# Optimization experiments

Measured on AMD Instinct MI355X. Metric: run time of the kernel, lower is better.

## Reference

```python
import jax, jax.numpy as jnp
import numpy as np

NUM_USERS = 120000
NUM_ITEMS = 30000
NUM_NODES = NUM_USERS + NUM_ITEMS
EMBED_DIM = 64
N_LAYERS = 3
N_EDGES = 4000000


def setup_inputs() -> dict:
    key = jax.random.key(0)
    k_emb, k_row, k_col = jax.random.split(key, 3)
    row = jax.random.randint(k_row, (N_EDGES,), 0, NUM_NODES, dtype=jnp.int32)
    col = jax.random.randint(k_col, (N_EDGES,), 0, NUM_NODES, dtype=jnp.int32)
    # symmetric normalization weights: D^{-1/2}[row] * D^{-1/2}[col]
    deg = jnp.bincount(row, length=NUM_NODES).astype(jnp.float32)
    deg_inv_sqrt = jnp.where(deg > 0, deg ** -0.5, 0.0)
    edge_weight = deg_inv_sqrt[row] * deg_inv_sqrt[col]
    emb = 0.1 * jax.random.normal(k_emb, (NUM_NODES, EMBED_DIM), dtype=jnp.float32)
    return {"emb": emb, "edge_weight": edge_weight, "row": row, "col": col}


def reference(emb, edge_weight, row, col):
    # one LightGCN propagation: out[row] += edge_weight * x[col]  (SpMM)
    def propagate(x):
        msg = x[col] * edge_weight[:, None]            # [E, D] gather + scale
        return jax.ops.segment_sum(msg, row, num_segments=NUM_NODES)  # scatter-add

    out = emb
    xk = emb
    for _ in range(N_LAYERS):
        xk = propagate(xk)
        out = out + xk
    out = out / (N_LAYERS + 1)
    user_emb = out[:NUM_USERS]
    item_emb = out[NUM_USERS:]
    return (user_emb, item_emb)
```

## Files before the change

### kernel.cpp

```cpp
#include <hip/hip_runtime.h>

#define NUM_USERS 120000
#define NUM_ITEMS 30000
#define NUM_NODES 150000
#define EMBED_DIM 64
#define N_LAYERS 3
#define N_EDGES 4000000

#define BW_SHIFT 9
#define BW_ROWS (1 << BW_SHIFT)
#define BW_MASK (BW_ROWS - 1)
#define NBUCK ((NUM_NODES + BW_MASK) >> BW_SHIFT)
#define BUCK_CAP 16000


__device__ __forceinline__ float bf2f(unsigned short u) {
    union { unsigned int i; float f; } v;
    v.i = ((unsigned int)u) << 16;
    return v.f;
}
__device__ __forceinline__ unsigned short f2bf(float f) {
    union { float f; unsigned int i; } v;
    v.f = f;
    unsigned int u = v.i;
    u += 0x7FFFu + ((u >> 16) & 1u);
    return (unsigned short)(u >> 16);
}


__global__ void zero_ints(int* __restrict__ p, int n) {
    int i = blockIdx.x * blockDim.x + threadIdx.x;
    int stride = gridDim.x * blockDim.x;
    for (; i < n; i += stride) p[i] = 0;
}

__global__ void conv_bf(const float4* __restrict__ src, ushort4* __restrict__ dst,
                        int n4) {
    int i = blockIdx.x * blockDim.x + threadIdx.x;
    int stride = gridDim.x * blockDim.x;
    for (; i < n4; i += stride) {
        float4 v = src[i];
        ushort4 q;
        q.x = f2bf(v.x); q.y = f2bf(v.y); q.z = f2bf(v.z); q.w = f2bf(v.w);
        dst[i] = q;
    }
}


__global__ void bucket_bin(const int* __restrict__ row, const int* __restrict__ col,
                           const float* __restrict__ w,
                           int* __restrict__ gcnt, int2* __restrict__ stage,
                           int nEdges) {
    __shared__ int cnt[NBUCK];
    __shared__ int bbase[NBUCK];
    int tile = (nEdges + gridDim.x - 1) / gridDim.x;
    int t0 = blockIdx.x * tile;
    int t1 = t0 + tile;
    if (t1 > nEdges) t1 = nEdges;
    for (int j = threadIdx.x; j < NBUCK; j += blockDim.x) cnt[j] = 0;
    __syncthreads();
    for (int i = t0 + threadIdx.x; i < t1; i += blockDim.x)
        atomicAdd(&cnt[row[i] >> BW_SHIFT], 1);
    __syncthreads();
    for (int j = threadIdx.x; j < NBUCK; j += blockDim.x) {
        int c = cnt[j];
        bbase[j] = c ? atomicAdd(&gcnt[j], c) : 0;
        cnt[j] = 0;
    }
    __syncthreads();
    for (int i = t0 + threadIdx.x; i < t1; i += blockDim.x) {
        int r = row[i];
        int b = r >> BW_SHIFT;
        int rank = bbase[b] + atomicAdd(&cnt[b], 1);
        if (rank < BUCK_CAP)
            stage[(size_t)b * BUCK_CAP + rank] =
                make_int2(((r & BW_MASK) << 18) | col[i], __float_as_int(w[i]));
    }
}

__global__ void bucket_scan(const int* __restrict__ gcnt, int* __restrict__ bstart,
                            int* __restrict__ rs) {
    __shared__ int s0[512], s1[512];
    int tid = threadIdx.x;
    int v = 0;
    if (tid < NBUCK) { v = gcnt[tid]; if (v > BUCK_CAP) v = BUCK_CAP; }
    s0[tid] = v;
    __syncthreads();
    int* a = s0; int* bb = s1;
    for (int off = 1; off < 512; off <<= 1) {
        int x = a[tid];
        if (tid >= off) x += a[tid - off];
        bb[tid] = x;
        __syncthreads();
        int* t = a; a = bb; bb = t;
    }
    if (tid == 0) bstart[0] = 0;
    if (tid < NBUCK) bstart[tid + 1] = a[tid];
    if (tid == 0) rs[NUM_NODES] = a[NBUCK - 1];
}

__global__ void __launch_bounds__(256)
bucket_scatter(const int2* __restrict__ stage, const int* __restrict__ gcnt,
               const int* __restrict__ bstart, int* __restrict__ rs,
               int2* __restrict__ csr) {
    __shared__ int s0[BW_ROWS], s1[BW_ROWS];
    int b = blockIdx.x;
    int tid = threadIdx.x;
    int nrec = gcnt[b]; if (nrec > BUCK_CAP) nrec = BUCK_CAP;
    int base = bstart[b];
    const int2* st = stage + (size_t)b * BUCK_CAP;
    int baseRow = b << BW_SHIFT;
    int rows = NUM_NODES - baseRow; if (rows > BW_ROWS) rows = BW_ROWS;

    for (int j = tid; j < BW_ROWS; j += 256) s0[j] = 0;
    __syncthreads();
    for (int i = tid; i < nrec; i += 256) atomicAdd(&s0[st[i].x >> 18], 1);
    __syncthreads();

    int* a = s0; int* bb = s1;
    for (int off = 1; off < BW_ROWS; off <<= 1) {
        for (int j = tid; j < BW_ROWS; j += 256) {
            int x = a[j];
            if (j >= off) x += a[j - off];
            bb[j] = x;
        }
        __syncthreads();
        int* t = a; a = bb; bb = t;
    }

    for (int r = tid; r < rows; r += 256)
        rs[baseRow + r] = base + (r ? a[r - 1] : 0);

    for (int j = tid; j < BW_ROWS; j += 256) bb[j] = 0;
    __syncthreads();
    for (int i = tid; i < nrec; i += 256) {
        int2 rec = st[i];
        int r = rec.x >> 18;
        int rank = atomicAdd(&bb[r], 1);
        csr[base + (r ? a[r - 1] : 0) + rank] = make_int2(rec.x & 0x3FFFF, rec.y);
    }
}

__global__ void lgcn_prop_bf(const ushort4* __restrict__ xb,
                             const int* __restrict__ rs,
                             const int2* __restrict__ csr,
                             ushort4* __restrict__ yb,
                             const float4* __restrict__ addIn,
                             float4* __restrict__ out,
                             float scale, int nNodes, int writeY) {
    int gtid = blockIdx.x * blockDim.x + threadIdx.x;
    int node = gtid >> 4;
    int sub  = threadIdx.x & 15;
    if (node >= nNodes) return;
    int s = rs[node], e = rs[node + 1];
    float4 acc = make_float4(0.f, 0.f, 0.f, 0.f);

    int base = s;
    for (; base + 16 <= e; base += 16) {
        int2 cw = csr[base + sub];
#pragma unroll
        for (int j = 0; j < 16; ++j) {
            int bc   = __shfl(cw.x, j, 16);
            float bw = __int_as_float(__shfl(cw.y, j, 16));
            ushort4 v = xb[(size_t)bc * 16 + sub];
            acc.x = fmaf(bf2f(v.x), bw, acc.x);
            acc.y = fmaf(bf2f(v.y), bw, acc.y);
            acc.z = fmaf(bf2f(v.z), bw, acc.z);
            acc.w = fmaf(bf2f(v.w), bw, acc.w);
        }
    }
    if (base < e) {
        int idx = base + sub;
        int2 cw = (idx < e) ? csr[idx] : make_int2(0, 0);
        int nn = e - base;
        for (int j = 0; j < nn; ++j) {
            int bc   = __shfl(cw.x, j, 16);
            float bw = __int_as_float(__shfl(cw.y, j, 16));
            ushort4 v = xb[(size_t)bc * 16 + sub];
            acc.x = fmaf(bf2f(v.x), bw, acc.x);
            acc.y = fmaf(bf2f(v.y), bw, acc.y);
            acc.z = fmaf(bf2f(v.z), bw, acc.z);
            acc.w = fmaf(bf2f(v.w), bw, acc.w);
        }
    }

    size_t o = (size_t)node * 16 + sub;
    if (writeY) {
        ushort4 q;
        q.x = f2bf(acc.x); q.y = f2bf(acc.y); q.z = f2bf(acc.z); q.w = f2bf(acc.w);
        yb[o] = q;
    }
    float4 a = addIn[o];
    a.x = (a.x + acc.x) * scale;
    a.y = (a.y + acc.y) * scale;
    a.z = (a.z + acc.z) * scale;
    a.w = (a.w + acc.w) * scale;
    out[o] = a;
}


__global__ void lgcn_init(const float4* __restrict__ emb,
                          float4* __restrict__ x,
                          float4* __restrict__ out, int n4) {
    int i = blockIdx.x * blockDim.x + threadIdx.x;
    int stride = gridDim.x * blockDim.x;
    for (; i < n4; i += stride) {
        float4 v = emb[i];
        x[i] = v;
        out[i] = v;
    }
}

__global__ void lgcn_zero(float4* __restrict__ y, int n4) {
    int i = blockIdx.x * blockDim.x + threadIdx.x;
    int stride = gridDim.x * blockDim.x;
    float4 z = make_float4(0.f, 0.f, 0.f, 0.f);
    for (; i < n4; i += stride) y[i] = z;
}

__global__ void lgcn_edge(const float* __restrict__ x,
                          const float* __restrict__ w,
                          const int* __restrict__ row,
                          const int* __restrict__ col,
                          float* __restrict__ y, int nEdges) {
    int tid = blockIdx.x * blockDim.x + threadIdx.x;
    int wave = tid >> 6;
    int lane = threadIdx.x & 63;
    int nWaves = (gridDim.x * blockDim.x) >> 6;
    for (int e = wave; e < nEdges; e += nWaves) {
        int r = row[e];
        int c = col[e];
        float wt = w[e];
        float v = x[(size_t)c * EMBED_DIM + lane] * wt;
        atomicAdd(&y[(size_t)r * EMBED_DIM + lane], v);
    }
}

__global__ void lgcn_accum(const float4* __restrict__ y,
                           float4* __restrict__ out, float scale, int n4) {
    int i = blockIdx.x * blockDim.x + threadIdx.x;
    int stride = gridDim.x * blockDim.x;
    for (; i < n4; i += stride) {
        float4 o = out[i];
        float4 v = y[i];
        o.x = (o.x + v.x) * scale;
        o.y = (o.y + v.y) * scale;
        o.z = (o.z + v.z) * scale;
        o.w = (o.w + v.w) * scale;
        out[i] = o;
    }
}


extern "C" void kernel_launch(void* const* d_in, const int* in_sizes, int n_in,
                              void* d_out, int out_size, void* d_ws, size_t ws_size,
                              hipStream_t stream) {
    const float* emb = (const float*)d_in[0];
    const float* ew  = (const float*)d_in[1];
    const int*   row = (const int*)d_in[2];
    const int*   col = (const int*)d_in[3];
    float* out = (float*)d_out;

    const size_t tableElems = (size_t)NUM_NODES * EMBED_DIM;
    const int n4 = (int)(tableElems / 4);

    char* ws = (char*)d_ws;
    size_t off = 0;
    auto alloc = [&](size_t bytes) {
        char* p = ws + off;
        off += (bytes + 255) & ~(size_t)255;
        return p;
    };
    ushort4* yAb   = (ushort4*)alloc(tableElems * 2);
    ushort4* yBb   = (ushort4*)alloc(tableElems * 2);
    int2*    csr   = (int2*)   alloc((size_t)N_EDGES * 8);
    int2*    stage = (int2*)   alloc((size_t)NBUCK * BUCK_CAP * 8);
    int*     rs    = (int*)    alloc((size_t)(NUM_NODES + 32) * 4);
    int*     bstart= (int*)    alloc((size_t)(NBUCK + 8) * 4);
    int*     gcnt  = (int*)    alloc((size_t)(NBUCK + 8) * 4);
    size_t need = off;
    ushort4* embb = (ushort4*)stage;

    if (ws_size >= need) {
        zero_ints<<<2, 256, 0, stream>>>(gcnt, NBUCK);
        bucket_bin<<<512, 256, 0, stream>>>(row, col, ew, gcnt, stage, N_EDGES);
        bucket_scan<<<1, 512, 0, stream>>>(gcnt, bstart, rs);
        bucket_scatter<<<NBUCK, 256, 0, stream>>>(stage, gcnt, bstart, rs, csr);

        conv_bf<<<2048, 256, 0, stream>>>((const float4*)emb, (ushort4*)embb, n4);

        const int propBlocks = (NUM_NODES * 16 + 255) / 256;
        lgcn_prop_bf<<<propBlocks, 256, 0, stream>>>(embb, rs, csr, yAb,
                                                     (const float4*)emb,
                                                     (float4*)out,
                                                     1.0f, NUM_NODES, 1);
        lgcn_prop_bf<<<propBlocks, 256, 0, stream>>>(yAb, rs, csr, yBb,
                                                     (const float4*)out,
                                                     (float4*)out,
                                                     1.0f, NUM_NODES, 1);
        lgcn_prop_bf<<<propBlocks, 256, 0, stream>>>(yBb, rs, csr, yAb,
                                                     (const float4*)out,
                                                     (float4*)out,
                                                     1.0f / (N_LAYERS + 1),
                                                     NUM_NODES, 0);
    } else {
        float* x = (float*)d_ws;
        float* y = x + tableElems;
        lgcn_init<<<2048, 256, 0, stream>>>((const float4*)emb, (float4*)x,
                                            (float4*)out, n4);
        for (int l = 0; l < N_LAYERS; ++l) {
            lgcn_zero<<<2048, 256, 0, stream>>>((float4*)y, n4);
            lgcn_edge<<<4096, 256, 0, stream>>>(x, ew, row, col, y, N_EDGES);
            float scale = (l == N_LAYERS - 1) ? 1.0f / (N_LAYERS + 1) : 1.0f;
            lgcn_accum<<<2048, 256, 0, stream>>>((const float4*)y, (float4*)out,
                                                 scale, n4);
            float* t = x; x = y; y = t;
        }
    }
}
```

Baseline: 377.6 us.

## Locally sort edges in shared memory, widen SpMM gathers, use nontemporal accesses

The binning kernel now processes 4096-edge sub-tiles, sorting them by bucket in shared memory via a local prefix scan, so writes to the staging buffer land in contiguous runs instead of being scattered. The propagation kernel uses 8 lanes per node with 16-byte bf16 gathers instead of 16 lanes with 8-byte gathers, which halves the shuffles and doubles the bytes per load. Streaming CSR, output and staging traffic switches to nontemporal loads and stores so the gathered embedding table stays in cache. In exchange, each lane holds more registers, and the smaller lane group puts more serial edge work on each lane.

```diff
diff --git a/kernel.cpp b/kernel.cpp
--- a/kernel.cpp
+++ b/kernel.cpp
@@ -12,6 +12,10 @@
 #define BW_MASK (BW_ROWS - 1)
 #define NBUCK ((NUM_NODES + BW_MASK) >> BW_SHIFT)
 #define BUCK_CAP 16000
+#define SUB_E 4096
+
+typedef float  f4v  __attribute__((ext_vector_type(4)));
+typedef unsigned short us8v __attribute__((ext_vector_type(8)));
 
 
 __device__ __forceinline__ float bf2f(unsigned short u) {
@@ -26,6 +30,26 @@
     u += 0x7FFFu + ((u >> 16) & 1u);
     return (unsigned short)(u >> 16);
 }
+__device__ __forceinline__ int2 ntload_i2(const int2* p) {
+    union { long long l; int2 v; } u;
+    u.l = __builtin_nontemporal_load((const long long*)p);
+    return u.v;
+}
+__device__ __forceinline__ void ntstore_i2(int2* p, int2 v) {
+    union { long long l; int2 v; } u;
+    u.v = v;
+    __builtin_nontemporal_store(u.l, (long long*)p);
+}
+__device__ __forceinline__ float4 ntload_f4(const float4* p) {
+    union { f4v a; float4 b; } u;
+    u.a = __builtin_nontemporal_load((const f4v*)p);
+    return u.b;
+}
+__device__ __forceinline__ void ntstore_f4(float4* p, float4 v) {
+    union { f4v a; float4 b; } u;
+    u.b = v;
+    __builtin_nontemporal_store(u.a, (f4v*)p);
+}
 
 
 __global__ void zero_ints(int* __restrict__ p, int n) {
@@ -47,34 +71,64 @@
 }
 
 
-__global__ void bucket_bin(const int* __restrict__ row, const int* __restrict__ col,
-                           const float* __restrict__ w,
-                           int* __restrict__ gcnt, int2* __restrict__ stage,
-                           int nEdges) {
-    __shared__ int cnt[NBUCK];
-    __shared__ int bbase[NBUCK];
-    int tile = (nEdges + gridDim.x - 1) / gridDim.x;
-    int t0 = blockIdx.x * tile;
-    int t1 = t0 + tile;
-    if (t1 > nEdges) t1 = nEdges;
-    for (int j = threadIdx.x; j < NBUCK; j += blockDim.x) cnt[j] = 0;
-    __syncthreads();
-    for (int i = t0 + threadIdx.x; i < t1; i += blockDim.x)
-        atomicAdd(&cnt[row[i] >> BW_SHIFT], 1);
-    __syncthreads();
-    for (int j = threadIdx.x; j < NBUCK; j += blockDim.x) {
-        int c = cnt[j];
-        bbase[j] = c ? atomicAdd(&gcnt[j], c) : 0;
-        cnt[j] = 0;
-    }
-    __syncthreads();
-    for (int i = t0 + threadIdx.x; i < t1; i += blockDim.x) {
-        int r = row[i];
-        int b = r >> BW_SHIFT;
-        int rank = bbase[b] + atomicAdd(&cnt[b], 1);
-        if (rank < BUCK_CAP)
-            stage[(size_t)b * BUCK_CAP + rank] =
-                make_int2(((r & BW_MASK) << 18) | col[i], __float_as_int(w[i]));
+__global__ void __launch_bounds__(256)
+bucket_bin2(const int* __restrict__ row, const int* __restrict__ col,
+            const float* __restrict__ w,
+            int* __restrict__ gcnt, int2* __restrict__ stage, int nEdges) {
+    __shared__ int2 lbuf[SUB_E];
+    __shared__ int  ldst[SUB_E];
+    __shared__ int  hist[NBUCK];
+    __shared__ int  cur[NBUCK];
+    __shared__ int  dlt[NBUCK];
+    __shared__ int  s0[512], s1[512];
+
+    int nSub = (nEdges + SUB_E - 1) / SUB_E;
+    for (int s = blockIdx.x; s < nSub; s += gridDim.x) {
+        int e0 = s * SUB_E;
+        int n = nEdges - e0; if (n > SUB_E) n = SUB_E;
+
+        for (int j = threadIdx.x; j < NBUCK; j += 256) hist[j] = 0;
+        __syncthreads();
+        for (int i = threadIdx.x; i < n; i += 256)
+            atomicAdd(&hist[row[e0 + i] >> BW_SHIFT], 1);
+        __syncthreads();
+
+        for (int j = threadIdx.x; j < 512; j += 256)
+            s0[j] = (j < NBUCK) ? hist[j] : 0;
+        __syncthreads();
+        int *a = s0, *bb = s1;
+        for (int off = 1; off < 512; off <<= 1) {
+            for (int j = threadIdx.x; j < 512; j += 256) {
+                int x = a[j];
+                if (j >= off) x += a[j - off];
+                bb[j] = x;
+            }
+            __syncthreads();
+            int* t = a; a = bb; bb = t;
+        }
+        for (int j = threadIdx.x; j < NBUCK; j += 256) {
+            int c = hist[j];
+            int ls = j ? a[j - 1] : 0;
+            cur[j] = ls;
+            int g = c ? atomicAdd(&gcnt[j], c) : 0;
+            dlt[j] = j * BUCK_CAP + g - ls;
+        }
+        __syncthreads();
+        for (int i = threadIdx.x; i < n; i += 256) {
+            int r = row[e0 + i];
+            int b = r >> BW_SHIFT;
+            int lpos = atomicAdd(&cur[b], 1);
+            lbuf[lpos] = make_int2(((r & BW_MASK) << 18) | col[e0 + i],
+                                   __float_as_int(w[e0 + i]));
+            int d = dlt[b] + lpos;
+            ldst[lpos] = (d - b * BUCK_CAP < BUCK_CAP) ? d : -1;
+        }
+        __syncthreads();
+        for (int j = threadIdx.x; j < n; j += 256) {
+            int d = ldst[j];
+            if (d >= 0) ntstore_i2(&stage[d], lbuf[j]);
+        }
+        __syncthreads();
     }
 }
 
@@ -137,65 +191,73 @@
         int2 rec = st[i];
         int r = rec.x >> 18;
         int rank = atomicAdd(&bb[r], 1);
-        csr[base + (r ? a[r - 1] : 0) + rank] = make_int2(rec.x & 0x3FFFF, rec.y);
-    }
-}
-
-__global__ void lgcn_prop_bf(const ushort4* __restrict__ xb,
-                             const int* __restrict__ rs,
-                             const int2* __restrict__ csr,
-                             ushort4* __restrict__ yb,
-                             const float4* __restrict__ addIn,
-                             float4* __restrict__ out,
-                             float scale, int nNodes, int writeY) {
+        ntstore_i2(&csr[base + (r ? a[r - 1] : 0) + rank],
+                   make_int2(rec.x & 0x3FFFF, rec.y));
+    }
+}
+
+__global__ void __launch_bounds__(256)
+lgcn_prop_bf8(const us8v* __restrict__ xb,
+              const int* __restrict__ rs,
+              const int2* __restrict__ csr,
+              us8v* __restrict__ yb,
+              const float4* __restrict__ addIn,
+              float4* __restrict__ out,
+              float scale, int nNodes, int writeY) {
     int gtid = blockIdx.x * blockDim.x + threadIdx.x;
-    int node = gtid >> 4;
-    int sub  = threadIdx.x & 15;
+    int node = gtid >> 3;
+    int sub  = threadIdx.x & 7;
     if (node >= nNodes) return;
     int s = rs[node], e = rs[node + 1];
-    float4 acc = make_float4(0.f, 0.f, 0.f, 0.f);
+    float acc[8] = {0.f, 0.f, 0.f, 0.f, 0.f, 0.f, 0.f, 0.f};
 
     int base = s;
-    for (; base + 16 <= e; base += 16) {
-        int2 cw = csr[base + sub];
+    for (; base + 8 <= e; base += 8) {
+        int2 cw = ntload_i2(&csr[base + sub]);
 #pragma unroll
-        for (int j = 0; j < 16; ++j) {
-            int bc   = __shfl(cw.x, j, 16);
-            float bw = __int_as_float(__shfl(cw.y, j, 16));
-            ushort4 v = xb[(size_t)bc * 16 + sub];
-            acc.x = fmaf(bf2f(v.x), bw, acc.x);
-            acc.y = fmaf(bf2f(v.y), bw, acc.y);
-            acc.z = fmaf(bf2f(v.z), bw, acc.z);
-            acc.w = fmaf(bf2f(v.w), bw, acc.w);
+        for (int j = 0; j < 8; ++j) {
+            int bc   = __shfl(cw.x, j, 8);
+            float bw = __int_as_float(__shfl(cw.y, j, 8));
+            us8v v = xb[(size_t)bc * 8 + sub];
+#pragma unroll
+            for (int k = 0; k < 8; ++k)
+                acc[k] = fmaf(bf2f(v[k]), bw, acc[k]);
         }
     }
     if (base < e) {
         int idx = base + sub;
-        int2 cw = (idx < e) ? csr[idx] : make_int2(0, 0);
+        int2 cw = (idx < e) ? ntload_i2(&csr[idx]) : make_int2(0, 0);
         int nn = e - base;
         for (int j = 0; j < nn; ++j) {
-            int bc   = __shfl(cw.x, j, 16);
-            float bw = __int_as_float(__shfl(cw.y, j, 16));
-            ushort4 v = xb[(size_t)bc * 16 + sub];
-            acc.x = fmaf(bf2f(v.x), bw, acc.x);
-            acc.y = fmaf(bf2f(v.y), bw, acc.y);
-            acc.z = fmaf(bf2f(v.z), bw, acc.z);
-            acc.w = fmaf(bf2f(v.w), bw, acc.w);
-        }
-    }
-
-    size_t o = (size_t)node * 16 + sub;
+            int bc   = __shfl(cw.x, j, 8);
+            float bw = __int_as_float(__shfl(cw.y, j, 8));
+            us8v v = xb[(size_t)bc * 8 + sub];
+#pragma unroll
+            for (int k = 0; k < 8; ++k)
+                acc[k] = fmaf(bf2f(v[k]), bw, acc[k]);
+        }
+    }
+
+    size_t o8 = (size_t)node * 8 + sub;
     if (writeY) {
-        ushort4 q;
-        q.x = f2bf(acc.x); q.y = f2bf(acc.y); q.z = f2bf(acc.z); q.w = f2bf(acc.w);
-        yb[o] = q;
-    }
-    float4 a = addIn[o];
-    a.x = (a.x + acc.x) * scale;
-    a.y = (a.y + acc.y) * scale;
-    a.z = (a.z + acc.z) * scale;
-    a.w = (a.w + acc.w) * scale;
-    out[o] = a;
+        us8v q;
+#pragma unroll
+        for (int k = 0; k < 8; ++k) q[k] = f2bf(acc[k]);
+        __builtin_nontemporal_store(q, &yb[o8]);
+    }
+    size_t o4 = o8 * 2;
+    float4 a0 = ntload_f4(&addIn[o4]);
+    float4 a1 = ntload_f4(&addIn[o4 + 1]);
+    a0.x = (a0.x + acc[0]) * scale;
+    a0.y = (a0.y + acc[1]) * scale;
+    a0.z = (a0.z + acc[2]) * scale;
+    a0.w = (a0.w + acc[3]) * scale;
+    a1.x = (a1.x + acc[4]) * scale;
+    a1.y = (a1.y + acc[5]) * scale;
+    a1.z = (a1.z + acc[6]) * scale;
+    a1.w = (a1.w + acc[7]) * scale;
+    ntstore_f4(&out[o4], a0);
+    ntstore_f4(&out[o4 + 1], a1);
 }
 
 
@@ -283,26 +345,29 @@
 
     if (ws_size >= need) {
         zero_ints<<<2, 256, 0, stream>>>(gcnt, NBUCK);
-        bucket_bin<<<512, 256, 0, stream>>>(row, col, ew, gcnt, stage, N_EDGES);
+        bucket_bin2<<<512, 256, 0, stream>>>(row, col, ew, gcnt, stage, N_EDGES);
         bucket_scan<<<1, 512, 0, stream>>>(gcnt, bstart, rs);
         bucket_scatter<<<NBUCK, 256, 0, stream>>>(stage, gcnt, bstart, rs, csr);
 
         conv_bf<<<2048, 256, 0, stream>>>((const float4*)emb, (ushort4*)embb, n4);
 
-        const int propBlocks = (NUM_NODES * 16 + 255) / 256;
-        lgcn_prop_bf<<<propBlocks, 256, 0, stream>>>(embb, rs, csr, yAb,
-                                                     (const float4*)emb,
-                                                     (float4*)out,
-                                                     1.0f, NUM_NODES, 1);
-        lgcn_prop_bf<<<propBlocks, 256, 0, stream>>>(yAb, rs, csr, yBb,
-                                                     (const float4*)out,
-                                                     (float4*)out,
-                                                     1.0f, NUM_NODES, 1);
-        lgcn_prop_bf<<<propBlocks, 256, 0, stream>>>(yBb, rs, csr, yAb,
-                                                     (const float4*)out,
-                                                     (float4*)out,
-                                                     1.0f / (N_LAYERS + 1),
-                                                     NUM_NODES, 0);
+        const int propBlocks = (NUM_NODES * 8 + 255) / 256;
+        lgcn_prop_bf8<<<propBlocks, 256, 0, stream>>>((const us8v*)embb, rs, csr,
+                                                      (us8v*)yAb,
+                                                      (const float4*)emb,
+                                                      (float4*)out,
+                                                      1.0f, NUM_NODES, 1);
+        lgcn_prop_bf8<<<propBlocks, 256, 0, stream>>>((const us8v*)yAb, rs, csr,
+                                                      (us8v*)yBb,
+                                                      (const float4*)out,
+                                                      (float4*)out,
+                                                      1.0f, NUM_NODES, 1);
+        lgcn_prop_bf8<<<propBlocks, 256, 0, stream>>>((const us8v*)yBb, rs, csr,
+                                                      (us8v*)yAb,
+                                                      (const float4*)out,
+                                                      (float4*)out,
+                                                      1.0f / (N_LAYERS + 1),
+                                                      NUM_NODES, 0);
     } else {
         float* x = (float*)d_ws;
         float* y = x + tableElems;
```

Measured after the change: 500.5 us. +32.5%, slower.
